# Kernel tuning notes

Hardware: AMD Instinct MI355X
Metric: run time of the kernel (lower is better)

The kernel has to match this reference:

```python
import jax, jax.numpy as jnp
import numpy as np

DECAY = 0.9      # decay_rate l
LR = 0.5         # fast-weight learning_rate e
STEP = 3         # inner-loop iterations
EPS = 1e-3       # keras LayerNormalization default epsilon

B, D_IN, U = 128, 256, 512


def setup_inputs() -> dict:
    key = jax.random.key(0)
    ks = jax.random.split(key, 6)
    return {
        "inputs": jax.random.normal(ks[0], (B, D_IN), dtype=jnp.float32),
        "prev_state": jax.random.normal(ks[1], (B, U), dtype=jnp.float32),
        "A": jax.random.normal(ks[2], (B, U, U), dtype=jnp.float32) * 0.01,
        "C": jax.random.normal(ks[3], (D_IN, U), dtype=jnp.float32) * (1.0 / np.sqrt(D_IN)),
        # original: glorot-identity init scaled by 0.05; randomized here, same math
        "W_h": jax.random.normal(ks[4], (U, U), dtype=jnp.float32) * 0.05,
        "bias": jax.random.normal(ks[5], (U,), dtype=jnp.float32) * 0.01,
        "gamma": jnp.ones((U,), dtype=jnp.float32),
        "beta": jnp.zeros((U,), dtype=jnp.float32),
    }


def _layer_norm(x, gamma, beta):
    m = jnp.mean(x, axis=-1, keepdims=True)
    v = jnp.var(x, axis=-1, keepdims=True)
    return (x - m) * jax.lax.rsqrt(v + EPS) * gamma + beta


def reference(inputs, prev_state, A, C, W_h, bias, gamma, beta):
    # slow path: h = act(prev @ W_h + x @ C + b)   -> [B, U]
    pre = prev_state @ W_h + inputs @ C
    h = jnp.tanh(pre + bias)
    # fast-weight update: A' = l*A + e * outer(h, h)  -> [B, U, U]
    A_new = DECAY * A + LR * jnp.einsum("bi,bj->bij", h, h)
    # inner loop: h_s = LN(act(prelim + h_s @ A'))  with h_s: [B, 1, U]
    prelim = pre[:, None, :]          # no bias / no activation, matching source
    h_s = h[:, None, :]
    for _ in range(STEP):
        h_s = jnp.tanh(prelim + jnp.einsum("bku,buv->bkv", h_s, A_new))
        h_s = _layer_norm(h_s, gamma, beta)
    out = h_s[:, 0, :]                # [B, U]; also the new recurrent state
    return out, A_new
```

## Files before the change

kernel.cpp:

```cpp
#include <hip/hip_runtime.h>
#include <math.h>

#define UDIM 512
#define DIN  256
#define BATCH 128
#define EPSV 1e-3f

__global__ __launch_bounds__(256) void k_pre(
    const float* __restrict__ inputs, const float* __restrict__ prev,
    const float* __restrict__ C, const float* __restrict__ Wh,
    const float* __restrict__ bias, float* __restrict__ pre, float* __restrict__ h)
{
    const int b = blockIdx.x >> 1;
    const int v = ((blockIdx.x & 1) << 8) + threadIdx.x;

    __shared__ float sprev[UDIM];
    __shared__ float sinp[DIN];
    for (int i = threadIdx.x; i < UDIM; i += 256) sprev[i] = prev[b * UDIM + i];
    sinp[threadIdx.x] = inputs[b * DIN + threadIdx.x];
    __syncthreads();

    float acc = 0.f;
#pragma unroll 8
    for (int u = 0; u < UDIM; ++u) acc = fmaf(sprev[u], Wh[u * UDIM + v], acc);
#pragma unroll 8
    for (int i = 0; i < DIN; ++i)  acc = fmaf(sinp[i], C[i * UDIM + v], acc);

    pre[b * UDIM + v] = acc;
    h[b * UDIM + v]   = tanhf(acc + bias[v]);
}

__global__ __launch_bounds__(1024) void k_steps(
    const float* __restrict__ A, const float* __restrict__ pre,
    const float* __restrict__ h, const float* __restrict__ gamma,
    const float* __restrict__ beta, float* __restrict__ Anew,
    float* __restrict__ out)
{
    const int b    = blockIdx.x;
    const int t    = threadIdx.x;
    const int lane = t & 63;
    const int wave = t >> 6;
    const int vg   = t & 127;
    const int v0   = vg << 2;
    const int useg = t >> 7;

    __shared__ __align__(16) float sh[UDIM];
    __shared__ __align__(16) float sx[UDIM];
    __shared__ __align__(16) float spre[UDIM];
    __shared__ __align__(16) float spart[8][UDIM];
    __shared__ float sred[16];
    __shared__ float sbc[4];

    if (t < UDIM) {
        float hv = h[(size_t)b * UDIM + t];
        sh[t] = hv; sx[t] = hv;
        spre[t] = pre[(size_t)b * UDIM + t];
    }
    __syncthreads();

    const float4 hv4 = *(const float4*)(sh + v0);
    const float* __restrict__ Ab  = A    + (size_t)b * UDIM * UDIM;
    float*       __restrict__ Anb = Anew + (size_t)b * UDIM * UDIM;
    const size_t rowbase = (size_t)(useg * 64) * UDIM + v0;

    for (int step = 0; step < 3; ++step) {
        {
            float p = (t < UDIM) ? sx[t] * sh[t] : 0.f;
#pragma unroll
            for (int off = 32; off; off >>= 1) p += __shfl_xor(p, off, 64);
            if (lane == 0) sred[wave] = p;
            __syncthreads();
            if (t == 0) {
                float d = 0.f;
#pragma unroll
                for (int i = 0; i < 8; ++i) d += sred[i];
                sbc[2] = d;
            }
            __syncthreads();
        }

        float4 acc = make_float4(0.f, 0.f, 0.f, 0.f);
        if (step == 0) {
#pragma unroll 4
            for (int k = 0; k < 64; ++k) {
                const float4 a4 = *(const float4*)(Ab + rowbase + (size_t)k * UDIM);
                const float xu = sh[useg * 64 + k];
                acc.x = fmaf(xu, a4.x, acc.x);
                acc.y = fmaf(xu, a4.y, acc.y);
                acc.z = fmaf(xu, a4.z, acc.z);
                acc.w = fmaf(xu, a4.w, acc.w);
                const float s = 0.5f * xu;
                float4 an;
                an.x = fmaf(s, hv4.x, 0.9f * a4.x);
                an.y = fmaf(s, hv4.y, 0.9f * a4.y);
                an.z = fmaf(s, hv4.z, 0.9f * a4.z);
                an.w = fmaf(s, hv4.w, 0.9f * a4.w);
                *(float4*)(Anb + rowbase + (size_t)k * UDIM) = an;
            }
        } else {
#pragma unroll 4
            for (int k = 0; k < 64; ++k) {
                const float4 a4 = *(const float4*)(Ab + rowbase + (size_t)k * UDIM);
                const float xu = sx[useg * 64 + k];
                acc.x = fmaf(xu, a4.x, acc.x);
                acc.y = fmaf(xu, a4.y, acc.y);
                acc.z = fmaf(xu, a4.z, acc.z);
                acc.w = fmaf(xu, a4.w, acc.w);
            }
        }
        *(float4*)(&spart[useg][v0]) = acc;
        __syncthreads();

        float hs = 0.f;
        if (t < UDIM) {
            float y = 0.f;
#pragma unroll
            for (int s = 0; s < 8; ++s) y += spart[s][t];
            y = 0.9f * y + 0.5f * sbc[2] * sh[t];
            hs = tanhf(spre[t] + y);
            float s1 = hs, s2 = hs * hs;
#pragma unroll
            for (int off = 32; off; off >>= 1) {
                s1 += __shfl_xor(s1, off, 64);
                s2 += __shfl_xor(s2, off, 64);
            }
            if (lane == 0) { sred[wave] = s1; sred[8 + wave] = s2; }
        }
        __syncthreads();
        if (t == 0) {
            float m = 0.f, q = 0.f;
#pragma unroll
            for (int i = 0; i < 8; ++i) { m += sred[i]; q += sred[8 + i]; }
            m *= (1.f / UDIM);
            q = q * (1.f / UDIM) - m * m;
            sbc[0] = m;
            sbc[1] = rsqrtf(q + EPSV);
        }
        __syncthreads();
        if (t < UDIM) {
            float xn = (hs - sbc[0]) * sbc[1] * gamma[t] + beta[t];
            sx[t] = xn;
            if (step == 2) out[(size_t)b * UDIM + t] = xn;
        }
        __syncthreads();
    }
}

extern "C" void kernel_launch(void* const* d_in, const int* in_sizes, int n_in,
                              void* d_out, int out_size, void* d_ws, size_t ws_size,
                              hipStream_t stream) {
    const float* inputs = (const float*)d_in[0];
    const float* prev   = (const float*)d_in[1];
    const float* A      = (const float*)d_in[2];
    const float* C      = (const float*)d_in[3];
    const float* Wh     = (const float*)d_in[4];
    const float* bias   = (const float*)d_in[5];
    const float* gamma  = (const float*)d_in[6];
    const float* beta   = (const float*)d_in[7];

    float* out  = (float*)d_out;
    float* Anew = out + (size_t)BATCH * UDIM;

    float* pre = (float*)d_ws;
    float* h   = pre + (size_t)BATCH * UDIM;

    k_pre  <<<BATCH * 2, 256, 0, stream>>>(inputs, prev, C, Wh, bias, pre, h);
    k_steps<<<BATCH, 1024, 0, stream>>>(A, pre, h, gamma, beta, Anew, out);
}
```

Baseline: 121.3 us.

## Split fused inner-loop kernel into per-step multi-block matvec kernels

Replaces the single 128-block kernel, which ran all three inner steps per batch row, with a chain of kernels that each split a batch's 512 columns into 8 chunks, giving 1024 blocks per step. Layer-norm statistics are passed between launches as per-chunk partial sums. Steps 2 and 3 now read the freshly written A_new instead of recomputing it from A with a correction term, so the step-0 kernel computes the matvec directly from A_new. This adds launch overhead and two extra passes over the 128 MB A_new, which may now come from cache or HBM, in exchange for much higher occupancy and memory-level parallelism.

```diff
diff --git a/kernel.cpp b/kernel.cpp
--- a/kernel.cpp
+++ b/kernel.cpp
@@ -6,6 +6,11 @@
 #define BATCH 128
 #define EPSV 1e-3f
 
+#define NCH  8
+#define CHW  64
+#define NSEG 32
+#define SEGH 16
+
 __global__ __launch_bounds__(256) void k_pre(
     const float* __restrict__ inputs, const float* __restrict__ prev,
     const float* __restrict__ C, const float* __restrict__ Wh,
@@ -30,119 +35,161 @@
     h[b * UDIM + v]   = tanhf(acc + bias[v]);
 }
 
-__global__ __launch_bounds__(1024) void k_steps(
+__global__ __launch_bounds__(512) void k_mv0(
     const float* __restrict__ A, const float* __restrict__ pre,
-    const float* __restrict__ h, const float* __restrict__ gamma,
-    const float* __restrict__ beta, float* __restrict__ Anew,
+    const float* __restrict__ h, float* __restrict__ Anew,
+    float* __restrict__ hsout, float* __restrict__ pstat)
+{
+    const int bc   = blockIdx.x;
+    const int b    = bc >> 3;
+    const int ch   = bc & 7;
+    const int t    = threadIdx.x;
+    const int vg   = t & 15;
+    const int useg = t >> 4;
+
+    __shared__ __align__(16) float sh[UDIM];
+    __shared__ float spre[CHW];
+    __shared__ __align__(16) float spart[NSEG][CHW];
+
+    if (t < UDIM) sh[t] = h[(size_t)b * UDIM + t];
+    if (t < CHW)  spre[t] = pre[(size_t)b * UDIM + ch * CHW + t];
+    __syncthreads();
+
+    const int gv0 = ch * CHW + vg * 4;
+    const float4 hv4 = *(const float4*)(sh + gv0);
+    const float* __restrict__ Ab  = A    + ((size_t)b * UDIM + useg * SEGH) * UDIM + gv0;
+    float*       __restrict__ Anb = Anew + ((size_t)b * UDIM + useg * SEGH) * UDIM + gv0;
+
+    float4 acc = make_float4(0.f, 0.f, 0.f, 0.f);
+#pragma unroll 8
+    for (int k = 0; k < SEGH; ++k) {
+        const float4 a4 = *(const float4*)(Ab + (size_t)k * UDIM);
+        const float hu = sh[useg * SEGH + k];
+        const float s = 0.5f * hu;
+        float4 an;
+        an.x = fmaf(s, hv4.x, 0.9f * a4.x);
+        an.y = fmaf(s, hv4.y, 0.9f * a4.y);
+        an.z = fmaf(s, hv4.z, 0.9f * a4.z);
+        an.w = fmaf(s, hv4.w, 0.9f * a4.w);
+        *(float4*)(Anb + (size_t)k * UDIM) = an;
+        acc.x = fmaf(hu, an.x, acc.x);
+        acc.y = fmaf(hu, an.y, acc.y);
+        acc.z = fmaf(hu, an.z, acc.z);
+        acc.w = fmaf(hu, an.w, acc.w);
+    }
+    *(float4*)(&spart[useg][vg * 4]) = acc;
+    __syncthreads();
+
+    if (t < CHW) {
+        float y = 0.f;
+#pragma unroll
+        for (int s = 0; s < NSEG; ++s) y += spart[s][t];
+        const float hs = tanhf(spre[t] + y);
+        hsout[(size_t)b * UDIM + ch * CHW + t] = hs;
+        float s1 = hs, s2 = hs * hs;
+#pragma unroll
+        for (int off = 32; off; off >>= 1) {
+            s1 += __shfl_xor(s1, off, 64);
+            s2 += __shfl_xor(s2, off, 64);
+        }
+        if (t == 0) { pstat[bc * 2] = s1; pstat[bc * 2 + 1] = s2; }
+    }
+}
+
+__global__ __launch_bounds__(512) void k_mv(
+    const float* __restrict__ An, const float* __restrict__ pre,
+    const float* __restrict__ hsin, const float* __restrict__ pstin,
+    const float* __restrict__ gamma, const float* __restrict__ beta,
+    float* __restrict__ hsout, float* __restrict__ pstout)
+{
+    const int bc   = blockIdx.x;
+    const int b    = bc >> 3;
+    const int ch   = bc & 7;
+    const int t    = threadIdx.x;
+    const int vg   = t & 15;
+    const int useg = t >> 4;
+
+    __shared__ __align__(16) float sx[UDIM];
+    __shared__ float spre[CHW];
+    __shared__ __align__(16) float spart[NSEG][CHW];
+    __shared__ float sbc[2];
+
+    if (t == 0) {
+        float m = 0.f, q = 0.f;
+#pragma unroll
+        for (int i = 0; i < NCH; ++i) {
+            m += pstin[(b * NCH + i) * 2];
+            q += pstin[(b * NCH + i) * 2 + 1];
+        }
+        m *= (1.f / UDIM);
+        q = q * (1.f / UDIM) - m * m;
+        sbc[0] = m;
+        sbc[1] = rsqrtf(q + EPSV);
+    }
+    if (t < CHW) spre[t] = pre[(size_t)b * UDIM + ch * CHW + t];
+    __syncthreads();
+    if (t < UDIM) {
+        const float hv = hsin[(size_t)b * UDIM + t];
+        sx[t] = (hv - sbc[0]) * sbc[1] * gamma[t] + beta[t];
+    }
+    __syncthreads();
+
+    const int gv0 = ch * CHW + vg * 4;
+    const float* __restrict__ Ab = An + ((size_t)b * UDIM + useg * SEGH) * UDIM + gv0;
+
+    float4 acc = make_float4(0.f, 0.f, 0.f, 0.f);
+#pragma unroll 8
+    for (int k = 0; k < SEGH; ++k) {
+        const float4 a4 = *(const float4*)(Ab + (size_t)k * UDIM);
+        const float xu = sx[useg * SEGH + k];
+        acc.x = fmaf(xu, a4.x, acc.x);
+        acc.y = fmaf(xu, a4.y, acc.y);
+        acc.z = fmaf(xu, a4.z, acc.z);
+        acc.w = fmaf(xu, a4.w, acc.w);
+    }
+    *(float4*)(&spart[useg][vg * 4]) = acc;
+    __syncthreads();
+
+    if (t < CHW) {
+        float y = 0.f;
+#pragma unroll
+        for (int s = 0; s < NSEG; ++s) y += spart[s][t];
+        const float hs = tanhf(spre[t] + y);
+        hsout[(size_t)b * UDIM + ch * CHW + t] = hs;
+        float s1 = hs, s2 = hs * hs;
+#pragma unroll
+        for (int off = 32; off; off >>= 1) {
+            s1 += __shfl_xor(s1, off, 64);
+            s2 += __shfl_xor(s2, off, 64);
+        }
+        if (t == 0) { pstout[bc * 2] = s1; pstout[bc * 2 + 1] = s2; }
+    }
+}
+
+__global__ __launch_bounds__(512) void k_fin(
+    const float* __restrict__ hsin, const float* __restrict__ pstin,
+    const float* __restrict__ gamma, const float* __restrict__ beta,
     float* __restrict__ out)
 {
-    const int b    = blockIdx.x;
-    const int t    = threadIdx.x;
-    const int lane = t & 63;
-    const int wave = t >> 6;
-    const int vg   = t & 127;
-    const int v0   = vg << 2;
-    const int useg = t >> 7;
-
-    __shared__ __align__(16) float sh[UDIM];
-    __shared__ __align__(16) float sx[UDIM];
-    __shared__ __align__(16) float spre[UDIM];
-    __shared__ __align__(16) float spart[8][UDIM];
-    __shared__ float sred[16];
-    __shared__ float sbc[4];
-
+    const int b = blockIdx.x;
+    const int t = threadIdx.x;
+    __shared__ float sbc[2];
+    if (t == 0) {
+        float m = 0.f, q = 0.f;
+#pragma unroll
+        for (int i = 0; i < NCH; ++i) {
+            m += pstin[(b * NCH + i) * 2];
+            q += pstin[(b * NCH + i) * 2 + 1];
+        }
+        m *= (1.f / UDIM);
+        q = q * (1.f / UDIM) - m * m;
+        sbc[0] = m;
+        sbc[1] = rsqrtf(q + EPSV);
+    }
+    __syncthreads();
     if (t < UDIM) {
-        float hv = h[(size_t)b * UDIM + t];
-        sh[t] = hv; sx[t] = hv;
-        spre[t] = pre[(size_t)b * UDIM + t];
-    }
-    __syncthreads();
-
-    const float4 hv4 = *(const float4*)(sh + v0);
-    const float* __restrict__ Ab  = A    + (size_t)b * UDIM * UDIM;
-    float*       __restrict__ Anb = Anew + (size_t)b * UDIM * UDIM;
-    const size_t rowbase = (size_t)(useg * 64) * UDIM + v0;
-
-    for (int step = 0; step < 3; ++step) {
-        {
-            float p = (t < UDIM) ? sx[t] * sh[t] : 0.f;
-#pragma unroll
-            for (int off = 32; off; off >>= 1) p += __shfl_xor(p, off, 64);
-            if (lane == 0) sred[wave] = p;
-            __syncthreads();
-            if (t == 0) {
-                float d = 0.f;
-#pragma unroll
-                for (int i = 0; i < 8; ++i) d += sred[i];
-                sbc[2] = d;
-            }
-            __syncthreads();
-        }
-
-        float4 acc = make_float4(0.f, 0.f, 0.f, 0.f);
-        if (step == 0) {
-#pragma unroll 4
-            for (int k = 0; k < 64; ++k) {
-                const float4 a4 = *(const float4*)(Ab + rowbase + (size_t)k * UDIM);
-                const float xu = sh[useg * 64 + k];
-                acc.x = fmaf(xu, a4.x, acc.x);
-                acc.y = fmaf(xu, a4.y, acc.y);
-                acc.z = fmaf(xu, a4.z, acc.z);
-                acc.w = fmaf(xu, a4.w, acc.w);
-                const float s = 0.5f * xu;
-                float4 an;
-                an.x = fmaf(s, hv4.x, 0.9f * a4.x);
-                an.y = fmaf(s, hv4.y, 0.9f * a4.y);
-                an.z = fmaf(s, hv4.z, 0.9f * a4.z);
-                an.w = fmaf(s, hv4.w, 0.9f * a4.w);
-                *(float4*)(Anb + rowbase + (size_t)k * UDIM) = an;
-            }
-        } else {
-#pragma unroll 4
-            for (int k = 0; k < 64; ++k) {
-                const float4 a4 = *(const float4*)(Ab + rowbase + (size_t)k * UDIM);
-                const float xu = sx[useg * 64 + k];
-                acc.x = fmaf(xu, a4.x, acc.x);
-                acc.y = fmaf(xu, a4.y, acc.y);
-                acc.z = fmaf(xu, a4.z, acc.z);
-                acc.w = fmaf(xu, a4.w, acc.w);
-            }
-        }
-        *(float4*)(&spart[useg][v0]) = acc;
-        __syncthreads();
-
-        float hs = 0.f;
-        if (t < UDIM) {
-            float y = 0.f;
-#pragma unroll
-            for (int s = 0; s < 8; ++s) y += spart[s][t];
-            y = 0.9f * y + 0.5f * sbc[2] * sh[t];
-            hs = tanhf(spre[t] + y);
-            float s1 = hs, s2 = hs * hs;
-#pragma unroll
-            for (int off = 32; off; off >>= 1) {
-                s1 += __shfl_xor(s1, off, 64);
-                s2 += __shfl_xor(s2, off, 64);
-            }
-            if (lane == 0) { sred[wave] = s1; sred[8 + wave] = s2; }
-        }
-        __syncthreads();
-        if (t == 0) {
-            float m = 0.f, q = 0.f;
-#pragma unroll
-            for (int i = 0; i < 8; ++i) { m += sred[i]; q += sred[8 + i]; }
-            m *= (1.f / UDIM);
-            q = q * (1.f / UDIM) - m * m;
-            sbc[0] = m;
-            sbc[1] = rsqrtf(q + EPSV);
-        }
-        __syncthreads();
-        if (t < UDIM) {
-            float xn = (hs - sbc[0]) * sbc[1] * gamma[t] + beta[t];
-            sx[t] = xn;
-            if (step == 2) out[(size_t)b * UDIM + t] = xn;
-        }
-        __syncthreads();
+        const float hv = hsin[(size_t)b * UDIM + t];
+        out[(size_t)b * UDIM + t] = (hv - sbc[0]) * sbc[1] * gamma[t] + beta[t];
     }
 }
 
@@ -161,9 +208,16 @@
     float* out  = (float*)d_out;
     float* Anew = out + (size_t)BATCH * UDIM;
 
-    float* pre = (float*)d_ws;
-    float* h   = pre + (size_t)BATCH * UDIM;
-
-    k_pre  <<<BATCH * 2, 256, 0, stream>>>(inputs, prev, C, Wh, bias, pre, h);
-    k_steps<<<BATCH, 1024, 0, stream>>>(A, pre, h, gamma, beta, Anew, out);
-}
+    float* pre  = (float*)d_ws;
+    float* h    = pre  + (size_t)BATCH * UDIM;
+    float* hsA  = h    + (size_t)BATCH * UDIM;
+    float* hsB  = hsA  + (size_t)BATCH * UDIM;
+    float* pstA = hsB  + (size_t)BATCH * UDIM;
+    float* pstB = pstA + (size_t)BATCH * NCH * 2;
+
+    k_pre<<<BATCH * 2, 256, 0, stream>>>(inputs, prev, C, Wh, bias, pre, h);
+    k_mv0<<<BATCH * NCH, 512, 0, stream>>>(A, pre, h, Anew, hsA, pstA);
+    k_mv <<<BATCH * NCH, 512, 0, stream>>>(Anew, pre, hsA, pstA, gamma, beta, hsB, pstB);
+    k_mv <<<BATCH * NCH, 512, 0, stream>>>(Anew, pre, hsB, pstB, gamma, beta, hsA, pstA);
+    k_fin<<<BATCH, 512, 0, stream>>>(hsA, pstA, gamma, beta, out);
+}
```

Result: slower. 144.6 us (+19.2%).

## Split per-batch step kernel into row-segment matvec kernels across launches

Applied to the files above, without the earlier changes.

Replaces the single 128-block kernel, which ran all three inner steps per batch element, with a chain of launches. Each launch uses 1024 blocks, one per (batch, row segment), and writes partial matvec results to workspace; the next launch reduces the partials, applies tanh and layer norm, then does its own partial matvec. Steps 1 and 2 now read A_new (rebuilt from the just-written Anew) instead of deriving the product algebraically from A, and the first pass uses nontemporal loads. The aim is to fill the GPU far better than 128 blocks can. The costs are extra kernel launches, extra global traffic for the partials, and re-reading the 128 MB A_new twice.

```diff
diff --git a/kernel.cpp b/kernel.cpp
--- a/kernel.cpp
+++ b/kernel.cpp
@@ -6,6 +6,12 @@
 #define BATCH 128
 #define EPSV 1e-3f
 
+#define NRSEG 8
+#define RPB   64
+#define HALFR 32
+
+typedef float f4 __attribute__((ext_vector_type(4)));
+
 __global__ __launch_bounds__(256) void k_pre(
     const float* __restrict__ inputs, const float* __restrict__ prev,
     const float* __restrict__ C, const float* __restrict__ Wh,
@@ -30,120 +36,175 @@
     h[b * UDIM + v]   = tanhf(acc + bias[v]);
 }
 
-__global__ __launch_bounds__(1024) void k_steps(
-    const float* __restrict__ A, const float* __restrict__ pre,
-    const float* __restrict__ h, const float* __restrict__ gamma,
-    const float* __restrict__ beta, float* __restrict__ Anew,
+__global__ __launch_bounds__(256) void k_mv0(
+    const float* __restrict__ A, const float* __restrict__ h,
+    float* __restrict__ Anew, float* __restrict__ ypart)
+{
+    const int bc   = blockIdx.x;
+    const int b    = bc >> 3;
+    const int rs   = bc & 7;
+    const int t    = threadIdx.x;
+    const int vg   = t & 127;
+    const int col  = vg << 2;
+    const int half = t >> 7;
+
+    __shared__ __align__(16) float sh[UDIM];
+    __shared__ __align__(16) float spart[2][UDIM];
+
+    sh[t]       = h[(size_t)b * UDIM + t];
+    sh[t + 256] = h[(size_t)b * UDIM + t + 256];
+    __syncthreads();
+
+    const f4 hv4 = *(const f4*)(sh + col);
+    const int row0 = rs * RPB + half * HALFR;
+    const float* __restrict__ Ab  = A    + ((size_t)b * UDIM + row0) * UDIM + col;
+    float*       __restrict__ Anb = Anew + ((size_t)b * UDIM + row0) * UDIM + col;
+
+    f4 acc = {0.f, 0.f, 0.f, 0.f};
+#pragma unroll 8
+    for (int k = 0; k < HALFR; ++k) {
+        const f4 a4 = __builtin_nontemporal_load((const f4*)(Ab + (size_t)k * UDIM));
+        const float hu = sh[row0 + k];
+        const float s = 0.5f * hu;
+        f4 an;
+        an.x = fmaf(s, hv4.x, 0.9f * a4.x);
+        an.y = fmaf(s, hv4.y, 0.9f * a4.y);
+        an.z = fmaf(s, hv4.z, 0.9f * a4.z);
+        an.w = fmaf(s, hv4.w, 0.9f * a4.w);
+        *(f4*)(Anb + (size_t)k * UDIM) = an;
+        acc.x = fmaf(hu, an.x, acc.x);
+        acc.y = fmaf(hu, an.y, acc.y);
+        acc.z = fmaf(hu, an.z, acc.z);
+        acc.w = fmaf(hu, an.w, acc.w);
+    }
+    *(f4*)(&spart[half][col]) = acc;
+    __syncthreads();
+
+    {
+        const float y0 = spart[0][t]       + spart[1][t];
+        const float y1 = spart[0][t + 256] + spart[1][t + 256];
+        ypart[(size_t)bc * UDIM + t]       = y0;
+        ypart[(size_t)bc * UDIM + t + 256] = y1;
+    }
+}
+
+__global__ __launch_bounds__(256) void k_mv(
+    const float* __restrict__ An, const float* __restrict__ pre,
+    const float* __restrict__ ypin, const float* __restrict__ gamma,
+    const float* __restrict__ beta, float* __restrict__ ypout)
+{
+    const int bc   = blockIdx.x;
+    const int b    = bc >> 3;
+    const int rs   = bc & 7;
+    const int t    = threadIdx.x;
+    const int lane = t & 63;
+    const int wave = t >> 6;
+    const int vg   = t & 127;
+    const int col  = vg << 2;
+    const int half = t >> 7;
+
+    __shared__ __align__(16) float sx[UDIM];
+    __shared__ float shs[UDIM];
+    __shared__ __align__(16) float spart[2][UDIM];
+    __shared__ float sred[8];
+    __shared__ float sbc[2];
+
+    {
+        float y0 = 0.f, y1 = 0.f;
+#pragma unroll
+        for (int s = 0; s < NRSEG; ++s) {
+            y0 += ypin[((size_t)b * NRSEG + s) * UDIM + t];
+            y1 += ypin[((size_t)b * NRSEG + s) * UDIM + t + 256];
+        }
+        const float hs0 = tanhf(pre[(size_t)b * UDIM + t] + y0);
+        const float hs1 = tanhf(pre[(size_t)b * UDIM + t + 256] + y1);
+        shs[t] = hs0; shs[t + 256] = hs1;
+        float s1 = hs0 + hs1, s2 = hs0 * hs0 + hs1 * hs1;
+#pragma unroll
+        for (int off = 32; off; off >>= 1) {
+            s1 += __shfl_xor(s1, off, 64);
+            s2 += __shfl_xor(s2, off, 64);
+        }
+        if (lane == 0) { sred[wave] = s1; sred[4 + wave] = s2; }
+    }
+    __syncthreads();
+    if (t == 0) {
+        float m = sred[0] + sred[1] + sred[2] + sred[3];
+        float q = sred[4] + sred[5] + sred[6] + sred[7];
+        m *= (1.f / UDIM);
+        q = q * (1.f / UDIM) - m * m;
+        sbc[0] = m;
+        sbc[1] = rsqrtf(q + EPSV);
+    }
+    __syncthreads();
+    {
+        const float m = sbc[0], r = sbc[1];
+        sx[t]       = (shs[t]       - m) * r * gamma[t]       + beta[t];
+        sx[t + 256] = (shs[t + 256] - m) * r * gamma[t + 256] + beta[t + 256];
+    }
+    __syncthreads();
+
+    const int row0 = rs * RPB + half * HALFR;
+    const float* __restrict__ Ab = An + ((size_t)b * UDIM + row0) * UDIM + col;
+
+    f4 acc = {0.f, 0.f, 0.f, 0.f};
+#pragma unroll 8
+    for (int k = 0; k < HALFR; ++k) {
+        const f4 a4 = *(const f4*)(Ab + (size_t)k * UDIM);
+        const float xu = sx[row0 + k];
+        acc.x = fmaf(xu, a4.x, acc.x);
+        acc.y = fmaf(xu, a4.y, acc.y);
+        acc.z = fmaf(xu, a4.z, acc.z);
+        acc.w = fmaf(xu, a4.w, acc.w);
+    }
+    *(f4*)(&spart[half][col]) = acc;
+    __syncthreads();
+
+    {
+        const float y0 = spart[0][t]       + spart[1][t];
+        const float y1 = spart[0][t + 256] + spart[1][t + 256];
+        ypout[(size_t)bc * UDIM + t]       = y0;
+        ypout[(size_t)bc * UDIM + t + 256] = y1;
+    }
+}
+
+__global__ __launch_bounds__(512) void k_fin(
+    const float* __restrict__ pre, const float* __restrict__ ypin,
+    const float* __restrict__ gamma, const float* __restrict__ beta,
     float* __restrict__ out)
 {
     const int b    = blockIdx.x;
     const int t    = threadIdx.x;
     const int lane = t & 63;
     const int wave = t >> 6;
-    const int vg   = t & 127;
-    const int v0   = vg << 2;
-    const int useg = t >> 7;
-
-    __shared__ __align__(16) float sh[UDIM];
-    __shared__ __align__(16) float sx[UDIM];
-    __shared__ __align__(16) float spre[UDIM];
-    __shared__ __align__(16) float spart[8][UDIM];
+
     __shared__ float sred[16];
-    __shared__ float sbc[4];
-
-    if (t < UDIM) {
-        float hv = h[(size_t)b * UDIM + t];
-        sh[t] = hv; sx[t] = hv;
-        spre[t] = pre[(size_t)b * UDIM + t];
-    }
-    __syncthreads();
-
-    const float4 hv4 = *(const float4*)(sh + v0);
-    const float* __restrict__ Ab  = A    + (size_t)b * UDIM * UDIM;
-    float*       __restrict__ Anb = Anew + (size_t)b * UDIM * UDIM;
-    const size_t rowbase = (size_t)(useg * 64) * UDIM + v0;
-
-    for (int step = 0; step < 3; ++step) {
-        {
-            float p = (t < UDIM) ? sx[t] * sh[t] : 0.f;
-#pragma unroll
-            for (int off = 32; off; off >>= 1) p += __shfl_xor(p, off, 64);
-            if (lane == 0) sred[wave] = p;
-            __syncthreads();
-            if (t == 0) {
-                float d = 0.f;
-#pragma unroll
-                for (int i = 0; i < 8; ++i) d += sred[i];
-                sbc[2] = d;
-            }
-            __syncthreads();
-        }
-
-        float4 acc = make_float4(0.f, 0.f, 0.f, 0.f);
-        if (step == 0) {
-#pragma unroll 4
-            for (int k = 0; k < 64; ++k) {
-                const float4 a4 = *(const float4*)(Ab + rowbase + (size_t)k * UDIM);
-                const float xu = sh[useg * 64 + k];
-                acc.x = fmaf(xu, a4.x, acc.x);
-                acc.y = fmaf(xu, a4.y, acc.y);
-                acc.z = fmaf(xu, a4.z, acc.z);
-                acc.w = fmaf(xu, a4.w, acc.w);
-                const float s = 0.5f * xu;
-                float4 an;
-                an.x = fmaf(s, hv4.x, 0.9f * a4.x);
-                an.y = fmaf(s, hv4.y, 0.9f * a4.y);
-                an.z = fmaf(s, hv4.z, 0.9f * a4.z);
-                an.w = fmaf(s, hv4.w, 0.9f * a4.w);
-                *(float4*)(Anb + rowbase + (size_t)k * UDIM) = an;
-            }
-        } else {
-#pragma unroll 4
-            for (int k = 0; k < 64; ++k) {
-                const float4 a4 = *(const float4*)(Ab + rowbase + (size_t)k * UDIM);
-                const float xu = sx[useg * 64 + k];
-                acc.x = fmaf(xu, a4.x, acc.x);
-                acc.y = fmaf(xu, a4.y, acc.y);
-                acc.z = fmaf(xu, a4.z, acc.z);
-                acc.w = fmaf(xu, a4.w, acc.w);
-            }
-        }
-        *(float4*)(&spart[useg][v0]) = acc;
-        __syncthreads();
-
-        float hs = 0.f;
-        if (t < UDIM) {
-            float y = 0.f;
-#pragma unroll
-            for (int s = 0; s < 8; ++s) y += spart[s][t];
-            y = 0.9f * y + 0.5f * sbc[2] * sh[t];
-            hs = tanhf(spre[t] + y);
-            float s1 = hs, s2 = hs * hs;
-#pragma unroll
-            for (int off = 32; off; off >>= 1) {
-                s1 += __shfl_xor(s1, off, 64);
-                s2 += __shfl_xor(s2, off, 64);
-            }
-            if (lane == 0) { sred[wave] = s1; sred[8 + wave] = s2; }
-        }
-        __syncthreads();
-        if (t == 0) {
-            float m = 0.f, q = 0.f;
-#pragma unroll
-            for (int i = 0; i < 8; ++i) { m += sred[i]; q += sred[8 + i]; }
-            m *= (1.f / UDIM);
-            q = q * (1.f / UDIM) - m * m;
-            sbc[0] = m;
-            sbc[1] = rsqrtf(q + EPSV);
-        }
-        __syncthreads();
-        if (t < UDIM) {
-            float xn = (hs - sbc[0]) * sbc[1] * gamma[t] + beta[t];
-            sx[t] = xn;
-            if (step == 2) out[(size_t)b * UDIM + t] = xn;
-        }
-        __syncthreads();
-    }
+    __shared__ float sbc[2];
+
+    float y = 0.f;
+#pragma unroll
+    for (int s = 0; s < NRSEG; ++s) y += ypin[((size_t)b * NRSEG + s) * UDIM + t];
+    const float hs = tanhf(pre[(size_t)b * UDIM + t] + y);
+
+    float s1 = hs, s2 = hs * hs;
+#pragma unroll
+    for (int off = 32; off; off >>= 1) {
+        s1 += __shfl_xor(s1, off, 64);
+        s2 += __shfl_xor(s2, off, 64);
+    }
+    if (lane == 0) { sred[wave] = s1; sred[8 + wave] = s2; }
+    __syncthreads();
+    if (t == 0) {
+        float m = 0.f, q = 0.f;
+#pragma unroll
+        for (int i = 0; i < 8; ++i) { m += sred[i]; q += sred[8 + i]; }
+        m *= (1.f / UDIM);
+        q = q * (1.f / UDIM) - m * m;
+        sbc[0] = m;
+        sbc[1] = rsqrtf(q + EPSV);
+    }
+    __syncthreads();
+    out[(size_t)b * UDIM + t] = (hs - sbc[0]) * sbc[1] * gamma[t] + beta[t];
 }
 
 extern "C" void kernel_launch(void* const* d_in, const int* in_sizes, int n_in,
@@ -161,9 +222,14 @@
     float* out  = (float*)d_out;
     float* Anew = out + (size_t)BATCH * UDIM;
 
-    float* pre = (float*)d_ws;
-    float* h   = pre + (size_t)BATCH * UDIM;
-
-    k_pre  <<<BATCH * 2, 256, 0, stream>>>(inputs, prev, C, Wh, bias, pre, h);
-    k_steps<<<BATCH, 1024, 0, stream>>>(A, pre, h, gamma, beta, Anew, out);
-}
+    float* pre  = (float*)d_ws;
+    float* h    = pre  + (size_t)BATCH * UDIM;
+    float* ypA  = h    + (size_t)BATCH * UDIM;
+    float* ypB  = ypA  + (size_t)BATCH * NRSEG * UDIM;
+
+    k_pre<<<BATCH * 2, 256, 0, stream>>>(inputs, prev, C, Wh, bias, pre, h);
+    k_mv0<<<BATCH * NRSEG, 256, 0, stream>>>(A, h, Anew, ypA);
+    k_mv <<<BATCH * NRSEG, 256, 0, stream>>>(Anew, pre, ypA, gamma, beta, ypB);
+    k_mv <<<BATCH * NRSEG, 256, 0, stream>>>(Anew, pre, ypB, gamma, beta, ypA);
+    k_fin<<<BATCH, 512, 0, stream>>>(pre, ypA, gamma, beta, out);
+}
```

Result: slower. 132.7 us (+9.4%).

## Split A_new update into separate blocks and batch A loads in the step loop

Applied to the files above, without the earlier changes.

The launch grid doubles. The extra 128 blocks compute and write A_new on their own, using nontemporal loads and stores. The original 128 blocks now only run the three matvec-plus-layernorm steps, reading A in groups of eight float4 loads to keep more memory requests in flight. This puts work on roughly twice as many CUs and takes the A_new store traffic off the critical step-0 path. The cost is one extra full pass reading A. Smaller tweaks move pre, gamma and beta into registers and skip the final shared-memory write.

```diff
diff --git a/kernel.cpp b/kernel.cpp
--- a/kernel.cpp
+++ b/kernel.cpp
@@ -5,6 +5,8 @@
 #define DIN  256
 #define BATCH 128
 #define EPSV 1e-3f
+
+typedef float f4 __attribute__((ext_vector_type(4)));
 
 __global__ __launch_bounds__(256) void k_pre(
     const float* __restrict__ inputs, const float* __restrict__ prev,
@@ -30,38 +32,66 @@
     h[b * UDIM + v]   = tanhf(acc + bias[v]);
 }
 
-__global__ __launch_bounds__(1024) void k_steps(
+__global__ __launch_bounds__(1024) void k_main(
     const float* __restrict__ A, const float* __restrict__ pre,
     const float* __restrict__ h, const float* __restrict__ gamma,
     const float* __restrict__ beta, float* __restrict__ Anew,
     float* __restrict__ out)
 {
+    const int t    = threadIdx.x;
+    const int vg   = t & 127;
+    const int col  = vg << 2;
+    const int rseg = t >> 7;
+    const int row0 = rseg * 64;
+
+    if (blockIdx.x >= BATCH) {
+        const int b = blockIdx.x - BATCH;
+        __shared__ __align__(16) float wsh[UDIM];
+        if (t < UDIM) wsh[t] = h[(size_t)b * UDIM + t];
+        __syncthreads();
+        const f4 hv4 = *(const f4*)(wsh + col);
+        const float* __restrict__ Ab  = A    + ((size_t)b * UDIM + row0) * UDIM + col;
+        float*       __restrict__ Anb = Anew + ((size_t)b * UDIM + row0) * UDIM + col;
+        for (int g = 0; g < 8; ++g) {
+            f4 buf[8];
+#pragma unroll
+            for (int j = 0; j < 8; ++j)
+                buf[j] = __builtin_nontemporal_load(
+                    (const f4*)(Ab + (size_t)(g * 8 + j) * UDIM));
+#pragma unroll
+            for (int j = 0; j < 8; ++j) {
+                const float s = 0.5f * wsh[row0 + g * 8 + j];
+                f4 an;
+                an.x = fmaf(s, hv4.x, 0.9f * buf[j].x);
+                an.y = fmaf(s, hv4.y, 0.9f * buf[j].y);
+                an.z = fmaf(s, hv4.z, 0.9f * buf[j].z);
+                an.w = fmaf(s, hv4.w, 0.9f * buf[j].w);
+                __builtin_nontemporal_store(an, (f4*)(Anb + (size_t)(g * 8 + j) * UDIM));
+            }
+        }
+        return;
+    }
+
     const int b    = blockIdx.x;
-    const int t    = threadIdx.x;
     const int lane = t & 63;
     const int wave = t >> 6;
-    const int vg   = t & 127;
-    const int v0   = vg << 2;
-    const int useg = t >> 7;
 
     __shared__ __align__(16) float sh[UDIM];
     __shared__ __align__(16) float sx[UDIM];
-    __shared__ __align__(16) float spre[UDIM];
     __shared__ __align__(16) float spart[8][UDIM];
     __shared__ float sred[16];
     __shared__ float sbc[4];
 
+    float prereg = 0.f, gam = 0.f, bet = 0.f;
     if (t < UDIM) {
-        float hv = h[(size_t)b * UDIM + t];
+        const float hv = h[(size_t)b * UDIM + t];
         sh[t] = hv; sx[t] = hv;
-        spre[t] = pre[(size_t)b * UDIM + t];
+        prereg = pre[(size_t)b * UDIM + t];
+        gam = gamma[t]; bet = beta[t];
     }
     __syncthreads();
 
-    const float4 hv4 = *(const float4*)(sh + v0);
-    const float* __restrict__ Ab  = A    + (size_t)b * UDIM * UDIM;
-    float*       __restrict__ Anb = Anew + (size_t)b * UDIM * UDIM;
-    const size_t rowbase = (size_t)(useg * 64) * UDIM + v0;
+    const float* __restrict__ Ab = A + ((size_t)b * UDIM + row0) * UDIM + col;
 
     for (int step = 0; step < 3; ++step) {
         {
@@ -73,42 +103,28 @@
             if (t == 0) {
                 float d = 0.f;
 #pragma unroll
-                for (int i = 0; i < 8; ++i) d += sred[i];
+                for (int i = 0; i < 16; ++i) d += sred[i];
                 sbc[2] = d;
             }
             __syncthreads();
         }
 
-        float4 acc = make_float4(0.f, 0.f, 0.f, 0.f);
-        if (step == 0) {
-#pragma unroll 4
-            for (int k = 0; k < 64; ++k) {
-                const float4 a4 = *(const float4*)(Ab + rowbase + (size_t)k * UDIM);
-                const float xu = sh[useg * 64 + k];
-                acc.x = fmaf(xu, a4.x, acc.x);
-                acc.y = fmaf(xu, a4.y, acc.y);
-                acc.z = fmaf(xu, a4.z, acc.z);
-                acc.w = fmaf(xu, a4.w, acc.w);
-                const float s = 0.5f * xu;
-                float4 an;
-                an.x = fmaf(s, hv4.x, 0.9f * a4.x);
-                an.y = fmaf(s, hv4.y, 0.9f * a4.y);
-                an.z = fmaf(s, hv4.z, 0.9f * a4.z);
-                an.w = fmaf(s, hv4.w, 0.9f * a4.w);
-                *(float4*)(Anb + rowbase + (size_t)k * UDIM) = an;
-            }
-        } else {
-#pragma unroll 4
-            for (int k = 0; k < 64; ++k) {
-                const float4 a4 = *(const float4*)(Ab + rowbase + (size_t)k * UDIM);
-                const float xu = sx[useg * 64 + k];
-                acc.x = fmaf(xu, a4.x, acc.x);
-                acc.y = fmaf(xu, a4.y, acc.y);
-                acc.z = fmaf(xu, a4.z, acc.z);
-                acc.w = fmaf(xu, a4.w, acc.w);
+        f4 acc = {0.f, 0.f, 0.f, 0.f};
+        for (int g = 0; g < 8; ++g) {
+            f4 buf[8];
+#pragma unroll
+            for (int j = 0; j < 8; ++j)
+                buf[j] = *(const f4*)(Ab + (size_t)(g * 8 + j) * UDIM);
+#pragma unroll
+            for (int j = 0; j < 8; ++j) {
+                const float xu = sx[row0 + g * 8 + j];
+                acc.x = fmaf(xu, buf[j].x, acc.x);
+                acc.y = fmaf(xu, buf[j].y, acc.y);
+                acc.z = fmaf(xu, buf[j].z, acc.z);
+                acc.w = fmaf(xu, buf[j].w, acc.w);
             }
         }
-        *(float4*)(&spart[useg][v0]) = acc;
+        *(f4*)(&spart[rseg][col]) = acc;
         __syncthreads();
 
         float hs = 0.f;
@@ -116,8 +132,8 @@
             float y = 0.f;
 #pragma unroll
             for (int s = 0; s < 8; ++s) y += spart[s][t];
-            y = 0.9f * y + 0.5f * sbc[2] * sh[t];
-            hs = tanhf(spre[t] + y);
+            y = fmaf(0.9f, y, 0.5f * sbc[2] * sh[t]);
+            hs = tanhf(prereg + y);
             float s1 = hs, s2 = hs * hs;
 #pragma unroll
             for (int off = 32; off; off >>= 1) {
@@ -138,9 +154,9 @@
         }
         __syncthreads();
         if (t < UDIM) {
-            float xn = (hs - sbc[0]) * sbc[1] * gamma[t] + beta[t];
-            sx[t] = xn;
+            const float xn = (hs - sbc[0]) * sbc[1] * gam + bet;
             if (step == 2) out[(size_t)b * UDIM + t] = xn;
+            else           sx[t] = xn;
         }
         __syncthreads();
     }
@@ -164,6 +180,6 @@
     float* pre = (float*)d_ws;
     float* h   = pre + (size_t)BATCH * UDIM;
 
-    k_pre  <<<BATCH * 2, 256, 0, stream>>>(inputs, prev, C, Wh, bias, pre, h);
-    k_steps<<<BATCH, 1024, 0, stream>>>(A, pre, h, gamma, beta, Anew, out);
+    k_pre <<<BATCH * 2, 256, 0, stream>>>(inputs, prev, C, Wh, bias, pre, h);
+    k_main<<<BATCH * 2, 1024, 0, stream>>>(A, pre, h, gamma, beta, Anew, out);
 }
```

Measured after the change: 179.7 us. +48.1%, slower.
